# Kernel tuning notes

Hardware: AMD Instinct MI355X
Metric: run time of the kernel (lower is better)

The kernel has to match this reference:

```python
import jax, jax.numpy as jnp
import numpy as np

N_PER_G = 100  # nodes per graph


def setup_inputs() -> dict:
    key = jax.random.key(0)
    ks = jax.random.split(key, 12)
    N, G, E = 100000, 1000, 1600000
    ninp, nout, K, H, H2 = 3, 10, 5, 64, 32
    x = jax.random.normal(ks[0], (N, ninp), jnp.float32)
    # within-graph random edges (contiguous node blocks per graph)
    epg = E // G
    gid = jnp.arange(E, dtype=jnp.int32) // epg
    src = jax.random.randint(ks[1], (E,), 0, N_PER_G, jnp.int32) + gid * N_PER_G
    dst = jax.random.randint(ks[2], (E,), 0, N_PER_G, jnp.int32) + gid * N_PER_G
    edge_index = jnp.stack([src, dst])
    batch = (jnp.arange(N, dtype=jnp.int32) // N_PER_G)
    lambda_max = 1.5 + 0.5 * jax.random.uniform(ks[3], (G,), jnp.float32)
    s = 0.05
    W1 = jax.random.normal(ks[4], (K, ninp, H), jnp.float32) * s
    b1 = jnp.zeros((H,), jnp.float32)
    W2 = jax.random.normal(ks[5], (K, H, H), jnp.float32) * s
    b2 = jnp.zeros((H,), jnp.float32)
    W3 = jax.random.normal(ks[6], (K, H, H), jnp.float32) * s
    b3 = jnp.zeros((H,), jnp.float32)
    bn_gamma = jnp.ones((H,), jnp.float32)
    bn_beta = jnp.zeros((H,), jnp.float32)
    bn_mean = jnp.zeros((H,), jnp.float32)
    bn_var = jnp.ones((H,), jnp.float32)
    fc1_w = jax.random.normal(ks[7], (H, H2), jnp.float32) * s
    fc1_b = jnp.zeros((H2,), jnp.float32)
    fc2_w = jax.random.normal(ks[8], (H2, nout), jnp.float32) * s
    fc2_b = jnp.zeros((nout,), jnp.float32)
    return dict(x=x, edge_index=edge_index, batch=batch, lambda_max=lambda_max,
                W1=W1, b1=b1, W2=W2, b2=b2, W3=W3, b3=b3,
                bn_gamma=bn_gamma, bn_beta=bn_beta, bn_mean=bn_mean, bn_var=bn_var,
                fc1_w=fc1_w, fc1_b=fc1_b, fc2_w=fc2_w, fc2_b=fc2_b)


def _cheb_conv(x, W, b, row, col, coef_edge, coef_loop):
    # PyG ChebConv with sym-normalized scaled Laplacian:
    # Lhat x = scatter_add(coef_edge * x[col] -> row) + coef_loop * x
    N = x.shape[0]
    def lhat(h):
        return jax.ops.segment_sum(coef_edge[:, None] * h[col], row,
                                   num_segments=N) + coef_loop[:, None] * h
    Tx0 = x
    out = Tx0 @ W[0]
    Tx1 = lhat(x)
    out = out + Tx1 @ W[1]
    for k in range(2, W.shape[0]):
        Tx2 = 2.0 * lhat(Tx1) - Tx0
        out = out + Tx2 @ W[k]
        Tx0, Tx1 = Tx1, Tx2
    return out + b


def reference(x, edge_index, batch, lambda_max,
              W1, b1, W2, b2, W3, b3,
              bn_gamma, bn_beta, bn_mean, bn_var,
              fc1_w, fc1_b, fc2_w, fc2_b):
    N = x.shape[0]
    G = lambda_max.shape[0]
    row, col = edge_index[0], edge_index[1]
    # sym Laplacian normalization, scaled by 2/lambda_max (per-graph)
    deg = jax.ops.segment_sum(jnp.ones_like(row, dtype=x.dtype), row, num_segments=N)
    dis = jnp.where(deg > 0, deg, 1.0) ** -0.5
    dis = jnp.where(deg > 0, dis, 0.0)
    lmax_e = lambda_max[batch[row]]
    coef_edge = -(2.0 / lmax_e) * dis[row] * dis[col]   # off-diagonal of Lhat
    coef_loop = 2.0 / lambda_max[batch] - 1.0           # diagonal of Lhat
    h = jax.nn.relu(_cheb_conv(x, W1, b1, row, col, coef_edge, coef_loop))
    h = jax.nn.relu(_cheb_conv(h, W2, b2, row, col, coef_edge, coef_loop))
    h = jax.nn.relu(_cheb_conv(h, W3, b3, row, col, coef_edge, coef_loop))
    # global mean pool over graphs
    sums = jax.ops.segment_sum(h, batch, num_segments=G)
    cnts = jax.ops.segment_sum(jnp.ones((N,), h.dtype), batch, num_segments=G)
    g = sums / jnp.maximum(cnts, 1.0)[:, None]
    # BatchNorm1d (eval mode, running stats), eps=1e-5
    g = (g - bn_mean) * jax.lax.rsqrt(bn_var + 1e-5) * bn_gamma + bn_beta
    g = jax.nn.relu(g @ fc1_w + fc1_b)
    return jax.nn.log_softmax(g @ fc2_w + fc2_b, axis=1)
```

## Files before the change

### kernel.cpp

```cpp
#include <hip/hip_runtime.h>
#include <hip/hip_bf16.h>

#define NPG 100
#define HF 64
#define NROW 128
#define ST 72
#define SAT 136
#define CMW 28

typedef float  f4   __attribute__((ext_vector_type(4)));
typedef float  f16v __attribute__((ext_vector_type(16)));
typedef short  bf8  __attribute__((ext_vector_type(8)));

#define SZ_TC  (HF * SAT * 2)
#define SZ_TRM (NROW * ST * 2)
#define OFF_TC  0
#define OFF_TRM SZ_TC
#define OFF_CM  0
#define OFF_MISC (OFF_TRM + SZ_TRM)
#define SMEM_BYTES (OFF_MISC + 1280)

#define WT_TOTAL 46080

__device__ __forceinline__ unsigned short f2bf(float f) {
    unsigned u = __float_as_uint(f);
    u += 0x7fffu + ((u >> 16) & 1u);
    return (unsigned short)(u >> 16);
}
__device__ __forceinline__ unsigned pk2bf(float a, float b) {
    float2 f2; f2.x = a; f2.y = b;
    __hip_bfloat162 h2 = __float22bfloat162_rn(f2);
    return *reinterpret_cast<unsigned*>(&h2);
}
__device__ __forceinline__ f16v zerov16() {
    f16v z;
    #pragma unroll
    for (int i = 0; i < 16; i++) z[i] = 0.f;
    return z;
}

__global__ void wconv(const float* __restrict__ W1, const float* __restrict__ W2,
                      const float* __restrict__ W3, unsigned short* __restrict__ ws)
{
    int idx = blockIdx.x * 256 + threadIdx.x;
    if (idx >= WT_TOTAL) return;
    float v;
    if (idx < 5120) {
        int k5 = idx >> 10, rem = idx & 1023, fo = rem >> 4, fi = rem & 15;
        v = (fi < 3) ? W1[(k5 * 3 + fi) * HF + fo] : 0.f;
    } else if (idx < 25600) {
        int j = idx - 5120;
        int k5 = j >> 12, rem = j & 4095, fo = rem >> 6, fi = rem & 63;
        v = W2[(k5 * HF + fi) * HF + fo];
    } else {
        int j = idx - 25600;
        int k5 = j >> 12, rem = j & 4095, fo = rem >> 6, fi = rem & 63;
        v = W3[(k5 * HF + fi) * HF + fo];
    }
    ws[idx] = f2bf(v);
}

__launch_bounds__(256, 2)
__global__ void chebpk(const float* __restrict__ x, const int* __restrict__ ei,
                       const float* __restrict__ lambda_max,
                       const unsigned short* __restrict__ Wt,
                       const float* __restrict__ b1, const float* __restrict__ b2,
                       const float* __restrict__ b3,
                       const float* __restrict__ bng, const float* __restrict__ bnb,
                       const float* __restrict__ bnm, const float* __restrict__ bnv,
                       const float* __restrict__ fc1w, const float* __restrict__ fc1b,
                       const float* __restrict__ fc2w, const float* __restrict__ fc2b,
                       float* __restrict__ out, int E_total, int epg)
{
    extern __shared__ char sm[];
    const int tid = threadIdx.x;
    const int g = blockIdx.x;
    const int ebase = g * epg, nbase = g * NPG;
    const int wg = tid >> 6, lane = tid & 63;
    const int l31 = lane & 31, hh = lane >> 5;
    const int ht  = wg & 1;
    const int Mt0 = (wg >> 1) * 2;
    const int fo  = ht * 32 + l31;

    unsigned* Cm  = (unsigned*)(sm + OFF_CM);
    float* dis    = (float*)(sm + OFF_MISC);
    float* pool   = (float*)(sm + OFF_MISC + 448);
    float* gvn    = (float*)(sm + OFF_MISC + 704);
    float* zf     = (float*)(sm + OFF_MISC + 960);
    float* logits = (float*)(sm + OFF_MISC + 1088);
    float* lsep   = (float*)(sm + OFF_MISC + 1152);

    const float lam = lambda_max[g];
    const float two_l = 2.0f / lam;
    const float cl = two_l - 1.0f;

    for (int i = tid; i < (NROW * CMW) / 4; i += 256)
        ((f4*)Cm)[i] = (f4){0.f, 0.f, 0.f, 0.f};
    __syncthreads();
    for (int e = tid; e < epg; e += 256) {
        int r = ei[ebase + e] - nbase;
        int c = ei[E_total + ebase + e] - nbase;
        atomicAdd(&Cm[r * CMW + (c >> 2)], 1u << (8 * (c & 3)));
    }
    __syncthreads();
    if (tid < 112) {
        float dv = 0.f;
        if (tid < NPG) {
            unsigned s = 0;
            #pragma unroll
            for (int w = 0; w < CMW; w++) {
                unsigned u = Cm[tid * CMW + w];
                s += (u & 255) + ((u >> 8) & 255) + ((u >> 16) & 255) + (u >> 24);
            }
            dv = s > 0 ? rsqrtf((float)s) : 0.f;
        }
        dis[tid] = dv;
    }
    __syncthreads();

    bf8 af[2][7];
    #pragma unroll
    for (int m = 0; m < 2; m++) {
        int rr = 32 * (Mt0 + m) + l31;
        bool rv = (rr < NPG);
        float base = rv ? (-two_l * dis[rr]) : 0.f;
        #pragma unroll
        for (int Ks = 0; Ks < 7; Ks++) {
            int k0 = Ks * 16 + 8 * hh;
            unsigned w0 = rv ? Cm[rr * CMW + (k0 >> 2)]     : 0u;
            unsigned w1 = rv ? Cm[rr * CMW + (k0 >> 2) + 1] : 0u;
            unsigned up[4];
            #pragma unroll
            for (int jj = 0; jj < 4; jj++) {
                int ka = k0 + 2 * jj, kb = ka + 1;
                unsigned wa = (jj < 2) ? w0 : w1;
                float va = base * (float)((wa >> (8 * (ka & 3))) & 255u) * dis[ka];
                float vb = base * (float)((wa >> (8 * (kb & 3))) & 255u) * dis[kb];
                if (rv && ka == rr) va += cl;
                if (rv && kb == rr) vb += cl;
                up[jj] = pk2bf(va, vb);
            }
            af[m][Ks] = *reinterpret_cast<bf8*>(up);
        }
    }
    __syncthreads();

    for (int i = tid; i < (SZ_TC + SZ_TRM) / 16; i += 256)
        ((f4*)sm)[i] = (f4){0.f, 0.f, 0.f, 0.f};
    if (tid < HF) pool[tid] = 0.f;
    __syncthreads();
    if (tid < NPG) {
        unsigned short h0 = f2bf(x[(nbase + tid) * 3 + 0]);
        unsigned short h1 = f2bf(x[(nbase + tid) * 3 + 1]);
        unsigned short h2 = f2bf(x[(nbase + tid) * 3 + 2]);
        *(unsigned*)(sm + OFF_TRM + (tid * ST) * 2) = (unsigned)h0 | ((unsigned)h1 << 16);
        *(unsigned short*)(sm + OFF_TRM + (tid * ST + 2) * 2) = h2;
        *(unsigned short*)(sm + OFF_TC + (0 * SAT + tid) * 2) = h0;
        *(unsigned short*)(sm + OFF_TC + (1 * SAT + tid) * 2) = h1;
        *(unsigned short*)(sm + OFF_TC + (2 * SAT + tid) * 2) = h2;
    }
    __syncthreads();

    f16v acc[2];
    unsigned prev[2][8], oldr[2][8];
    const float* bsv[3] = {b1, b2, b3};

    #pragma unroll
    for (int m = 0; m < 2; m++) {
        unsigned short tv[16];
        #pragma unroll
        for (int r = 0; r < 16; r++) {
            int np = (Mt0 + m) * 32 + (r & 3) + 8 * (r >> 2) + 4 * hh;
            tv[r] = *(const unsigned short*)(sm + OFF_TRM + (np * ST + fo) * 2);
        }
        #pragma unroll
        for (int p = 0; p < 8; p++)
            prev[m][p] = (unsigned)tv[2 * p] | ((unsigned)tv[2 * p + 1] << 16);
    }

    for (int L = 0; L < 3; L++) {
        const bool l1 = (L == 0);
        const unsigned short* Wl = l1 ? Wt : (Wt + (L == 1 ? 5120 : 25600));
        acc[0] = zerov16();
        acc[1] = zerov16();

        auto TW = [&](int k5) {
            const int nKs = l1 ? 1 : 4;
            for (int Ks = 0; Ks < nKs; Ks++) {
                bf8 bw;
                if (l1) bw = *(const bf8*)(Wl + (k5 * 64 + fo) * 16 + 8 * hh);
                else    bw = *(const bf8*)(Wl + (k5 * 64 + fo) * 64 + Ks * 16 + 8 * hh);
                #pragma unroll
                for (int m = 0; m < 2; m++) {
                    bf8 a = *(const bf8*)(sm + OFF_TRM +
                              (((Mt0 + m) * 32 + l31) * ST + Ks * 16 + 8 * hh) * 2);
                    acc[m] = __builtin_amdgcn_mfma_f32_32x32x16_bf16(a, bw, acc[m], 0, 0, 0);
                }
            }
        };

        TW(0);
        #pragma unroll
        for (int s = 1; s <= 4; s++) {
            bf8 bfr[7];
            #pragma unroll
            for (int Ks = 0; Ks < 7; Ks++)
                bfr[Ks] = *(const bf8*)(sm + OFF_TC + (fo * SAT + Ks * 16 + 8 * hh) * 2);
            __syncthreads();
            #pragma unroll
            for (int m = 0; m < 2; m++) {
                f16v c = zerov16();
                #pragma unroll
                for (int Ks = 0; Ks < 7; Ks++)
                    c = __builtin_amdgcn_mfma_f32_32x32x16_bf16(af[m][Ks], bfr[Ks], c, 0, 0, 0);
                unsigned hp[8];
                #pragma unroll
                for (int p = 0; p < 8; p++) {
                    float c0 = c[2 * p], c1 = c[2 * p + 1];
                    if (s >= 2) {
                        float olo = __uint_as_float(oldr[m][p] << 16);
                        float ohi = __uint_as_float(oldr[m][p] & 0xffff0000u);
                        c0 = 2.f * c0 - olo;
                        c1 = 2.f * c1 - ohi;
                    }
                    hp[p] = pk2bf(c0, c1);
                    if (s < 4) {
                        oldr[m][p] = prev[m][p];
                        prev[m][p] = hp[p];
                    }
                }
                if (s < 4) {
                    #pragma unroll
                    for (int q4 = 0; q4 < 4; q4++) {
                        int np0 = (Mt0 + m) * 32 + 8 * q4 + 4 * hh;
                        uint2 pk;
                        pk.x = hp[2 * q4];
                        pk.y = hp[2 * q4 + 1];
                        *(uint2*)(sm + OFF_TC + (fo * SAT + np0) * 2) = pk;
                    }
                }
                #pragma unroll
                for (int r = 0; r < 16; r++) {
                    int np = (Mt0 + m) * 32 + (r & 3) + 8 * (r >> 2) + 4 * hh;
                    unsigned short hv = (r & 1) ? (unsigned short)(hp[r >> 1] >> 16)
                                                : (unsigned short)(hp[r >> 1] & 0xffffu);
                    *(unsigned short*)(sm + OFF_TRM + (np * ST + fo) * 2) = hv;
                }
            }
            __syncthreads();
            TW(s);
        }
        __syncthreads();

        const float bias = bsv[L][fo];
        if (L < 2) {
            #pragma unroll
            for (int m = 0; m < 2; m++) {
                unsigned hp[8];
                #pragma unroll
                for (int p = 0; p < 8; p++) {
                    float v0 = fmaxf(acc[m][2 * p]     + bias, 0.f);
                    float v1 = fmaxf(acc[m][2 * p + 1] + bias, 0.f);
                    hp[p] = pk2bf(v0, v1);
                    prev[m][p] = hp[p];
                }
                #pragma unroll
                for (int q4 = 0; q4 < 4; q4++) {
                    int np0 = (Mt0 + m) * 32 + 8 * q4 + 4 * hh;
                    uint2 pk;
                    pk.x = hp[2 * q4];
                    pk.y = hp[2 * q4 + 1];
                    *(uint2*)(sm + OFF_TC + (fo * SAT + np0) * 2) = pk;
                }
                #pragma unroll
                for (int r = 0; r < 16; r++) {
                    int np = (Mt0 + m) * 32 + (r & 3) + 8 * (r >> 2) + 4 * hh;
                    unsigned short hv = (r & 1) ? (unsigned short)(hp[r >> 1] >> 16)
                                                : (unsigned short)(hp[r >> 1] & 0xffffu);
                    *(unsigned short*)(sm + OFF_TRM + (np * ST + fo) * 2) = hv;
                }
            }
            __syncthreads();
        } else {
            float ssum = 0.f;
            #pragma unroll
            for (int m = 0; m < 2; m++) {
                #pragma unroll
                for (int r = 0; r < 16; r++) {
                    int np = (Mt0 + m) * 32 + (r & 3) + 8 * (r >> 2) + 4 * hh;
                    float h = fmaxf(acc[m][r] + bias, 0.f);
                    if (np < NPG) ssum += h;
                }
            }
            ssum += __shfl_xor(ssum, 32, 64);
            if (hh == 0) atomicAdd(&pool[fo], ssum);
            __syncthreads();
        }
    }

    if (tid < HF) {
        float gv = pool[tid] * (1.0f / NPG);
        gv = (gv - bnm[tid]) * rsqrtf(bnv[tid] + 1e-5f) * bng[tid] + bnb[tid];
        gvn[tid] = gv;
    }
    __syncthreads();
    if (tid < 32) {
        float a = fc1b[tid];
        for (int f = 0; f < HF; f++) a += gvn[f] * fc1w[f * 32 + tid];
        zf[tid] = fmaxf(a, 0.f);
    }
    __syncthreads();
    if (tid < 10) {
        float a = fc2b[tid];
        for (int k = 0; k < 32; k++) a += zf[k] * fc2w[k * 10 + tid];
        logits[tid] = a;
    }
    __syncthreads();
    if (tid == 0) {
        float m = logits[0];
        for (int i = 1; i < 10; i++) m = fmaxf(m, logits[i]);
        float s = 0.f;
        for (int i = 0; i < 10; i++) s += expf(logits[i] - m);
        lsep[0] = m + logf(s);
    }
    __syncthreads();
    if (tid < 10) out[g * 10 + tid] = logits[tid] - lsep[0];
}

extern "C" void kernel_launch(void* const* d_in, const int* in_sizes, int n_in,
                              void* d_out, int out_size, void* d_ws, size_t ws_size,
                              hipStream_t stream) {
    const float* x    = (const float*)d_in[0];
    const int*   ei   = (const int*)d_in[1];
    const float* lmax = (const float*)d_in[3];
    const float* W1   = (const float*)d_in[4];
    const float* b1   = (const float*)d_in[5];
    const float* W2   = (const float*)d_in[6];
    const float* b2   = (const float*)d_in[7];
    const float* W3   = (const float*)d_in[8];
    const float* b3   = (const float*)d_in[9];
    const float* bng  = (const float*)d_in[10];
    const float* bnb  = (const float*)d_in[11];
    const float* bnm  = (const float*)d_in[12];
    const float* bnv  = (const float*)d_in[13];
    const float* fc1w = (const float*)d_in[14];
    const float* fc1b = (const float*)d_in[15];
    const float* fc2w = (const float*)d_in[16];
    const float* fc2b = (const float*)d_in[17];

    const int E = in_sizes[1] / 2;
    const int G = in_sizes[3];
    const int epg = E / G;

    unsigned short* Wt = (unsigned short*)d_ws;

    wconv<<<(WT_TOTAL + 255) / 256, 256, 0, stream>>>(W1, W2, W3, Wt);

    hipFuncSetAttribute((const void*)chebpk,
                        hipFuncAttributeMaxDynamicSharedMemorySize, SMEM_BYTES);

    chebpk<<<G, 256, SMEM_BYTES, stream>>>(x, ei, lmax, Wt, b1, b2, b3,
                                           bng, bnb, bnm, bnv, fc1w, fc1b, fc2w, fc2b,
                                           (float*)d_out, E, epg);
}
```

Measured before the change: 177.8 us.

## Give each wave full feature width and double-buffer transposed features to cut barriers

```diff
diff --git a/kernel.cpp b/kernel.cpp
--- a/kernel.cpp
+++ b/kernel.cpp
@@ -3,9 +3,8 @@
 
 #define NPG 100
 #define HF 64
-#define NROW 128
 #define ST 72
-#define SAT 136
+#define SAT 120
 #define CMW 28
 
 typedef float  f4   __attribute__((ext_vector_type(4)));
@@ -13,9 +12,10 @@
 typedef short  bf8  __attribute__((ext_vector_type(8)));
 
 #define SZ_TC  (HF * SAT * 2)
-#define SZ_TRM (NROW * ST * 2)
-#define OFF_TC  0
-#define OFF_TRM SZ_TC
+#define SZ_TRM (128 * ST * 2)
+#define OFF_TCA 0
+#define OFF_TCB SZ_TC
+#define OFF_TRM (2 * SZ_TC)
 #define OFF_CM  0
 #define OFF_MISC (OFF_TRM + SZ_TRM)
 #define SMEM_BYTES (OFF_MISC + 1280)
@@ -60,8 +60,8 @@
     ws[idx] = f2bf(v);
 }
 
-__launch_bounds__(256, 2)
-__global__ void chebpk(const float* __restrict__ x, const int* __restrict__ ei,
+__launch_bounds__(256, 1)
+__global__ void chebsw(const float* __restrict__ x, const int* __restrict__ ei,
                        const float* __restrict__ lambda_max,
                        const unsigned short* __restrict__ Wt,
                        const float* __restrict__ b1, const float* __restrict__ b2,
@@ -78,9 +78,6 @@
     const int ebase = g * epg, nbase = g * NPG;
     const int wg = tid >> 6, lane = tid & 63;
     const int l31 = lane & 31, hh = lane >> 5;
-    const int ht  = wg & 1;
-    const int Mt0 = (wg >> 1) * 2;
-    const int fo  = ht * 32 + l31;
 
     unsigned* Cm  = (unsigned*)(sm + OFF_CM);
     float* dis    = (float*)(sm + OFF_MISC);
@@ -94,7 +91,7 @@
     const float two_l = 2.0f / lam;
     const float cl = two_l - 1.0f;
 
-    for (int i = tid; i < (NROW * CMW) / 4; i += 256)
+    for (int i = tid; i < (128 * CMW) / 4; i += 256)
         ((f4*)Cm)[i] = (f4){0.f, 0.f, 0.f, 0.f};
     __syncthreads();
     for (int e = tid; e < epg; e += 256) {
@@ -118,10 +115,9 @@
     }
     __syncthreads();
 
-    bf8 af[2][7];
-    #pragma unroll
-    for (int m = 0; m < 2; m++) {
-        int rr = 32 * (Mt0 + m) + l31;
+    bf8 af[7];
+    {
+        int rr = 32 * wg + l31;
         bool rv = (rr < NPG);
         float base = rv ? (-two_l * dis[rr]) : 0.f;
         #pragma unroll
@@ -140,12 +136,12 @@
                 if (rv && kb == rr) vb += cl;
                 up[jj] = pk2bf(va, vb);
             }
-            af[m][Ks] = *reinterpret_cast<bf8*>(up);
+            af[Ks] = *reinterpret_cast<bf8*>(up);
         }
     }
     __syncthreads();
 
-    for (int i = tid; i < (SZ_TC + SZ_TRM) / 16; i += 256)
+    for (int i = tid; i < (2 * SZ_TC + SZ_TRM) / 16; i += 256)
         ((f4*)sm)[i] = (f4){0.f, 0.f, 0.f, 0.f};
     if (tid < HF) pool[tid] = 0.f;
     __syncthreads();
@@ -155,28 +151,15 @@
         unsigned short h2 = f2bf(x[(nbase + tid) * 3 + 2]);
         *(unsigned*)(sm + OFF_TRM + (tid * ST) * 2) = (unsigned)h0 | ((unsigned)h1 << 16);
         *(unsigned short*)(sm + OFF_TRM + (tid * ST + 2) * 2) = h2;
-        *(unsigned short*)(sm + OFF_TC + (0 * SAT + tid) * 2) = h0;
-        *(unsigned short*)(sm + OFF_TC + (1 * SAT + tid) * 2) = h1;
-        *(unsigned short*)(sm + OFF_TC + (2 * SAT + tid) * 2) = h2;
+        *(unsigned short*)(sm + OFF_TCA + (0 * SAT + tid) * 2) = h0;
+        *(unsigned short*)(sm + OFF_TCA + (1 * SAT + tid) * 2) = h1;
+        *(unsigned short*)(sm + OFF_TCA + (2 * SAT + tid) * 2) = h2;
     }
     __syncthreads();
 
     f16v acc[2];
-    unsigned prev[2][8], oldr[2][8];
     const float* bsv[3] = {b1, b2, b3};
-
-    #pragma unroll
-    for (int m = 0; m < 2; m++) {
-        unsigned short tv[16];
-        #pragma unroll
-        for (int r = 0; r < 16; r++) {
-            int np = (Mt0 + m) * 32 + (r & 3) + 8 * (r >> 2) + 4 * hh;
-            tv[r] = *(const unsigned short*)(sm + OFF_TRM + (np * ST + fo) * 2);
-        }
-        #pragma unroll
-        for (int p = 0; p < 8; p++)
-            prev[m][p] = (unsigned)tv[2 * p] | ((unsigned)tv[2 * p + 1] << 16);
-    }
+    const int arow = (32 * wg + l31) * ST;
 
     for (int L = 0; L < 3; L++) {
         const bool l1 = (L == 0);
@@ -187,113 +170,121 @@
         auto TW = [&](int k5) {
             const int nKs = l1 ? 1 : 4;
             for (int Ks = 0; Ks < nKs; Ks++) {
-                bf8 bw;
-                if (l1) bw = *(const bf8*)(Wl + (k5 * 64 + fo) * 16 + 8 * hh);
-                else    bw = *(const bf8*)(Wl + (k5 * 64 + fo) * 64 + Ks * 16 + 8 * hh);
-                #pragma unroll
-                for (int m = 0; m < 2; m++) {
-                    bf8 a = *(const bf8*)(sm + OFF_TRM +
-                              (((Mt0 + m) * 32 + l31) * ST + Ks * 16 + 8 * hh) * 2);
-                    acc[m] = __builtin_amdgcn_mfma_f32_32x32x16_bf16(a, bw, acc[m], 0, 0, 0);
+                bf8 a = *(const bf8*)(sm + OFF_TRM + (arow + Ks * 16 + 8 * hh) * 2);
+                #pragma unroll
+                for (int t = 0; t < 2; t++) {
+                    bf8 bw;
+                    if (l1) bw = *(const bf8*)(Wl + (k5 * 64 + 32 * t + l31) * 16 + 8 * hh);
+                    else    bw = *(const bf8*)(Wl + (k5 * 64 + 32 * t + l31) * 64 + Ks * 16 + 8 * hh);
+                    acc[t] = __builtin_amdgcn_mfma_f32_32x32x16_bf16(a, bw, acc[t], 0, 0, 0);
                 }
             }
         };
 
         TW(0);
+        int srcO = OFF_TCA, dstO = OFF_TCB;
         #pragma unroll
         for (int s = 1; s <= 4; s++) {
-            bf8 bfr[7];
-            #pragma unroll
-            for (int Ks = 0; Ks < 7; Ks++)
-                bfr[Ks] = *(const bf8*)(sm + OFF_TC + (fo * SAT + Ks * 16 + 8 * hh) * 2);
-            __syncthreads();
-            #pragma unroll
-            for (int m = 0; m < 2; m++) {
+            #pragma unroll
+            for (int t = 0; t < 2; t++) {
+                const int frow = (32 * t + l31) * SAT;
+                bf8 bfr[7];
+                #pragma unroll
+                for (int Ks = 0; Ks < 7; Ks++)
+                    bfr[Ks] = *(const bf8*)(sm + srcO + (frow + Ks * 16 + 8 * hh) * 2);
                 f16v c = zerov16();
                 #pragma unroll
                 for (int Ks = 0; Ks < 7; Ks++)
-                    c = __builtin_amdgcn_mfma_f32_32x32x16_bf16(af[m][Ks], bfr[Ks], c, 0, 0, 0);
+                    c = __builtin_amdgcn_mfma_f32_32x32x16_bf16(af[Ks], bfr[Ks], c, 0, 0, 0);
                 unsigned hp[8];
                 #pragma unroll
-                for (int p = 0; p < 8; p++) {
-                    float c0 = c[2 * p], c1 = c[2 * p + 1];
-                    if (s >= 2) {
-                        float olo = __uint_as_float(oldr[m][p] << 16);
-                        float ohi = __uint_as_float(oldr[m][p] & 0xffff0000u);
-                        c0 = 2.f * c0 - olo;
-                        c1 = 2.f * c1 - ohi;
-                    }
-                    hp[p] = pk2bf(c0, c1);
-                    if (s < 4) {
-                        oldr[m][p] = prev[m][p];
-                        prev[m][p] = hp[p];
-                    }
-                }
-                if (s < 4) {
+                for (int q4 = 0; q4 < 4; q4++) {
+                    int np0 = 32 * wg + 8 * q4 + 4 * hh;
+                    bool wv = (np0 < NPG);
+                    uint2 old;
+                    old.x = 0u; old.y = 0u;
+                    if (s >= 2 && wv)
+                        old = *(const uint2*)(sm + dstO + (frow + np0) * 2);
                     #pragma unroll
-                    for (int q4 = 0; q4 < 4; q4++) {
-                        int np0 = (Mt0 + m) * 32 + 8 * q4 + 4 * hh;
+                    for (int pp = 0; pp < 2; pp++) {
+                        int p = 2 * q4 + pp;
+                        unsigned ow = pp ? old.y : old.x;
+                        float c0 = c[2 * p], c1 = c[2 * p + 1];
+                        if (s >= 2) {
+                            c0 = 2.f * c0 - __uint_as_float(ow << 16);
+                            c1 = 2.f * c1 - __uint_as_float(ow & 0xffff0000u);
+                        }
+                        hp[p] = pk2bf(c0, c1);
+                    }
+                    if (s < 4 && wv) {
                         uint2 pk;
                         pk.x = hp[2 * q4];
                         pk.y = hp[2 * q4 + 1];
-                        *(uint2*)(sm + OFF_TC + (fo * SAT + np0) * 2) = pk;
+                        *(uint2*)(sm + dstO + (frow + np0) * 2) = pk;
                     }
                 }
                 #pragma unroll
                 for (int r = 0; r < 16; r++) {
-                    int np = (Mt0 + m) * 32 + (r & 3) + 8 * (r >> 2) + 4 * hh;
-                    unsigned short hv = (r & 1) ? (unsigned short)(hp[r >> 1] >> 16)
-                                                : (unsigned short)(hp[r >> 1] & 0xffffu);
-                    *(unsigned short*)(sm + OFF_TRM + (np * ST + fo) * 2) = hv;
-                }
-            }
-            __syncthreads();
+                    int np = 32 * wg + (r & 3) + 8 * (r >> 2) + 4 * hh;
+                    if (np < NPG) {
+                        unsigned short hv = (r & 1) ? (unsigned short)(hp[r >> 1] >> 16)
+                                                    : (unsigned short)(hp[r >> 1] & 0xffffu);
+                        *(unsigned short*)(sm + OFF_TRM + (np * ST + 32 * t + l31) * 2) = hv;
+                    }
+                }
+            }
             TW(s);
+            if (s < 4) __syncthreads();
+            int tmp = srcO; srcO = dstO; dstO = tmp;
         }
-        __syncthreads();
-
-        const float bias = bsv[L][fo];
+
         if (L < 2) {
             #pragma unroll
-            for (int m = 0; m < 2; m++) {
+            for (int t = 0; t < 2; t++) {
+                const float bias = bsv[L][32 * t + l31];
+                const int frow = (32 * t + l31) * SAT;
                 unsigned hp[8];
                 #pragma unroll
                 for (int p = 0; p < 8; p++) {
-                    float v0 = fmaxf(acc[m][2 * p]     + bias, 0.f);
-                    float v1 = fmaxf(acc[m][2 * p + 1] + bias, 0.f);
+                    float v0 = fmaxf(acc[t][2 * p]     + bias, 0.f);
+                    float v1 = fmaxf(acc[t][2 * p + 1] + bias, 0.f);
                     hp[p] = pk2bf(v0, v1);
-                    prev[m][p] = hp[p];
                 }
                 #pragma unroll
                 for (int q4 = 0; q4 < 4; q4++) {
-                    int np0 = (Mt0 + m) * 32 + 8 * q4 + 4 * hh;
-                    uint2 pk;
-                    pk.x = hp[2 * q4];
-                    pk.y = hp[2 * q4 + 1];
-                    *(uint2*)(sm + OFF_TC + (fo * SAT + np0) * 2) = pk;
+                    int np0 = 32 * wg + 8 * q4 + 4 * hh;
+                    if (np0 < NPG) {
+                        uint2 pk;
+                        pk.x = hp[2 * q4];
+                        pk.y = hp[2 * q4 + 1];
+                        *(uint2*)(sm + OFF_TCA + (frow + np0) * 2) = pk;
+                    }
                 }
                 #pragma unroll
                 for (int r = 0; r < 16; r++) {
-                    int np = (Mt0 + m) * 32 + (r & 3) + 8 * (r >> 2) + 4 * hh;
-                    unsigned short hv = (r & 1) ? (unsigned short)(hp[r >> 1] >> 16)
-                                                : (unsigned short)(hp[r >> 1] & 0xffffu);
-                    *(unsigned short*)(sm + OFF_TRM + (np * ST + fo) * 2) = hv;
+                    int np = 32 * wg + (r & 3) + 8 * (r >> 2) + 4 * hh;
+                    if (np < NPG) {
+                        unsigned short hv = (r & 1) ? (unsigned short)(hp[r >> 1] >> 16)
+                                                    : (unsigned short)(hp[r >> 1] & 0xffffu);
+                        *(unsigned short*)(sm + OFF_TRM + (np * ST + 32 * t + l31) * 2) = hv;
+                    }
                 }
             }
             __syncthreads();
         } else {
-            float ssum = 0.f;
-            #pragma unroll
-            for (int m = 0; m < 2; m++) {
+            #pragma unroll
+            for (int t = 0; t < 2; t++) {
+                const float bias = bsv[L][32 * t + l31];
+                float ssum = 0.f;
                 #pragma unroll
                 for (int r = 0; r < 16; r++) {
-                    int np = (Mt0 + m) * 32 + (r & 3) + 8 * (r >> 2) + 4 * hh;
-                    float h = fmaxf(acc[m][r] + bias, 0.f);
+                    int np = 32 * wg + (r & 3) + 8 * (r >> 2) + 4 * hh;
+                    float h = fmaxf(acc[t][r] + bias, 0.f);
                     if (np < NPG) ssum += h;
                 }
-            }
-            ssum += __shfl_xor(ssum, 32, 64);
-            if (hh == 0) atomicAdd(&pool[fo], ssum);
+                ssum += __shfl_xor(ssum, 32, 64);
+                if (hh == 0) atomicAdd(&pool[32 * t + l31], ssum);
+            }
             __syncthreads();
         }
     }
@@ -356,10 +347,10 @@
 
     wconv<<<(WT_TOTAL + 255) / 256, 256, 0, stream>>>(W1, W2, W3, Wt);
 
-    hipFuncSetAttribute((const void*)chebpk,
+    hipFuncSetAttribute((const void*)chebsw,
                         hipFuncAttributeMaxDynamicSharedMemorySize, SMEM_BYTES);
 
-    chebpk<<<G, 256, SMEM_BYTES, stream>>>(x, ei, lmax, Wt, b1, b2, b3,
+    chebsw<<<G, 256, SMEM_BYTES, stream>>>(x, ei, lmax, Wt, b1, b2, b3,
                                            bng, bnb, bnm, bnv, fc1w, fc1b, fc2w, fc2b,
                                            (float*)d_out, E, epg);
 }
```

Measured after the change: 190.6 us. 1.07x slower.
